# Optimization experiments

Hardware: AMD Instinct MI355X
Metric: run time of the kernel (lower is better)

Reference implementation:

```python
import jax, jax.numpy as jnp
import numpy as np
from jax import lax

EOS_ID = 2
START_ID = 1
NEG = -1e9
BEAM = 4
OUT_LEN = 48


def _lstm_gates(z):
    i, f, g, o = jnp.split(z, 4, axis=-1)
    return jax.nn.sigmoid(i), jax.nn.sigmoid(f), jnp.tanh(g), jax.nn.sigmoid(o)


def setup_inputs() -> dict:
    V, E, H, A = 32000, 512, 512, 512
    B, S_IN = 32, 128
    key = jax.random.key(0)
    ks = jax.random.split(key, 16)
    sd = 0.05
    n = lambda k, shp: jax.random.normal(k, shp, dtype=jnp.float32) * sd
    return {
        "encoder_inputs": jax.random.randint(ks[0], (B, S_IN), 0, V, dtype=jnp.int32),
        "decoder_inputs": jax.random.randint(ks[1], (B, OUT_LEN), 0, V, dtype=jnp.int32),
        "enc_emb": n(ks[2], (V, E)),
        "dec_emb": n(ks[3], (V, E)),
        "W_enc": n(ks[4], (E, 4 * H)),
        "U_enc": n(ks[5], (H, 4 * H)),
        "b_enc": jnp.zeros((4 * H,), jnp.float32),
        "W_dec": n(ks[6], (E + A, 4 * H)),
        "U_dec": n(ks[7], (H, 4 * H)),
        "b_dec": jnp.zeros((4 * H,), jnp.float32),
        "W_mem": n(ks[8], (H, A)),      # LuongAttention memory layer (no bias)
        "W_attn": n(ks[9], (2 * H, A)), # AttentionWrapper attention layer (no bias)
        "W_out": n(ks[10], (A, V)),
        "b_out": jnp.zeros((V,), jnp.float32),
    }


def reference(encoder_inputs, decoder_inputs, enc_emb, dec_emb, W_enc, U_enc, b_enc,
              W_dec, U_dec, b_dec, W_mem, W_attn, W_out, b_out):
    B = encoder_inputs.shape[0]
    H = U_enc.shape[0]
    A = W_mem.shape[1]
    V = W_out.shape[1]

    # ---- encoder LSTM (Keras gate order i,f,g,o) ----
    x = enc_emb[encoder_inputs]  # [B,S,E]
    def enc_step(carry, xt):
        h, c = carry
        i, f, g, o = _lstm_gates(xt @ W_enc + h @ U_enc + b_enc)
        c = f * c + i * g
        h = o * jnp.tanh(c)
        return (h, c), h
    h0 = jnp.zeros((B, H), x.dtype)
    (hN, cN), enc_out = lax.scan(enc_step, (h0, h0), x.transpose(1, 0, 2))
    enc_out = enc_out.transpose(1, 0, 2)       # [B,S,H] = attention values
    keys_mem = enc_out @ W_mem                 # [B,S,A] = attention keys

    # ---- beam search init (tile encoder final state over beams) ----
    h = jnp.broadcast_to(hN[:, None], (B, BEAM, H))
    c = jnp.broadcast_to(cN[:, None], (B, BEAM, H))
    attn = jnp.zeros((B, BEAM, A), x.dtype)
    cum = jnp.full((B, BEAM), NEG, x.dtype).at[:, 0].set(0.0)
    finished = jnp.zeros((B, BEAM), bool)
    tok = jnp.full((B, BEAM), START_ID, jnp.int32)
    eos_lp = jnp.full((V,), NEG, x.dtype).at[EOS_ID].set(0.0)

    def dec_step(carry, _):
        h, c, attn, cum, finished, tok = carry
        xe = dec_emb[tok]                                     # [B,K,E]
        inp = jnp.concatenate([xe, attn], axis=-1)            # cell_input_fn: concat(input, attention)
        i, f, g, o = _lstm_gates(inp @ W_dec + h @ U_dec + b_dec)
        c_new = f * c + i * g
        cell_out = o * jnp.tanh(c_new)                        # [B,K,H]
        scores = jnp.einsum('bkh,bsh->bks', cell_out, keys_mem)  # Luong dot score
        align = jax.nn.softmax(scores, axis=-1)
        ctx = jnp.einsum('bks,bsh->bkh', align, enc_out)
        attn_new = jnp.concatenate([cell_out, ctx], axis=-1) @ W_attn  # attention layer
        logits = attn_new @ W_out + b_out                     # [B,K,V]
        lp = jax.nn.log_softmax(logits, axis=-1)
        lp = jnp.where(finished[..., None], eos_lp, lp)       # finished beams repeat EOS
        total = cum[..., None] + lp
        vals, idx = lax.top_k(total.reshape(B, -1), BEAM)     # over K*V candidates
        parent = idx // V
        new_tok = (idx % V).astype(jnp.int32)
        g3 = lambda t: jnp.take_along_axis(t, parent[..., None], axis=1)
        h2 = g3(cell_out)
        c2 = g3(c_new)
        attn2 = g3(attn_new)
        fin = jnp.take_along_axis(finished, parent, axis=1) | (new_tok == EOS_ID)
        return (h2, c2, attn2, vals, fin, new_tok), (parent, new_tok)

    _, (parents, toks) = lax.scan(dec_step, (h, c, attn, cum, finished, tok), None, length=OUT_LEN)

    # ---- gather_tree: backtrack beam ancestry ----
    def back(ptr, pt):
        p, t = pt
        sel = jnp.take_along_axis(t, ptr, axis=1)
        return jnp.take_along_axis(p, ptr, axis=1), sel
    ptr0 = jnp.broadcast_to(jnp.arange(BEAM, dtype=jnp.int32)[None], (B, BEAM))
    _, pred = lax.scan(back, ptr0, (parents, toks), reverse=True)
    return pred.transpose(1, 0, 2)  # predicted_ids [B, T, beam]
```

## Files before the change

### kernel.cpp

```cpp
#include <hip/hip_runtime.h>
#include <math.h>

#define EOS_ID 2
#define START_ID 1
#define NEGV (-1e9f)

__device__ __forceinline__ float sigmoidf_(float x) { return 1.f / (1.f + expf(-x)); }

__device__ __forceinline__ void merge4_(float lv[4], int lc[4],
                                        const float rv[4], const int rc[4]) {
    float ov[4]; int oc[4];
    int ai = 0, bi = 0;
    #pragma unroll
    for (int o = 0; o < 4; o++) {
        const float avv = (ai == 0) ? lv[0] : (ai == 1) ? lv[1] : (ai == 2) ? lv[2] : lv[3];
        const int   acc = (ai == 0) ? lc[0] : (ai == 1) ? lc[1] : (ai == 2) ? lc[2] : lc[3];
        const float bvv = (bi == 0) ? rv[0] : (bi == 1) ? rv[1] : (bi == 2) ? rv[2] : rv[3];
        const int   bcc = (bi == 0) ? rc[0] : (bi == 1) ? rc[1] : (bi == 2) ? rc[2] : rc[3];
        const bool ta = (avv > bvv) || (avv == bvv && acc < bcc);
        ov[o] = ta ? avv : bvv;
        oc[o] = ta ? acc : bcc;
        if (ta) ai++; else bi++;
    }
    #pragma unroll
    for (int o = 0; o < 4; o++) { lv[o] = ov[o]; lc[o] = oc[o]; }
}

__device__ __forceinline__ void lse_combine_(float& m, float& s, float m2, float s2) {
    const float M = fmaxf(m, m2);
    s = s * expf(m - M) + s2 * expf(m2 - M);
    m = M;
}

template<int BM, int BN, int BK, int AMODE, int TRANS>
__global__ void __launch_bounds__(256) gemm_k(
    const float* __restrict__ A, const float* __restrict__ B,
    const float* __restrict__ bias, float* __restrict__ C,
    int M, int N, int K, const int* __restrict__ tokp)
{
    static_assert(BN == 64, "");
    constexpr int TM = BM / 16, TN = BN / 16;
    __shared__ __align__(16) float As[BK][BM];
    __shared__ __align__(16) float Bs[BK][BN];
    const int tid = threadIdx.x;
    const int n0 = blockIdx.x * BN, m0 = blockIdx.y * BM;
    const int tx = tid & 15, ty = tid >> 4;
    (void)M;

    float acc[TM][TN];
    #pragma unroll
    for (int i = 0; i < TM; i++)
        #pragma unroll
        for (int j = 0; j < TN; j++) acc[i][j] = 0.f;

    constexpr int A4 = BM * BK / 4;
    const bool aP = (A4 >= 256) || (tid < A4);
    const int am = tid / (BK / 4), ak4 = tid % (BK / 4);
    const int bk = tid >> 4, bn4 = tid & 15;

    const float* aRow = nullptr;
    if (aP) {
        if (AMODE == 0) {
            aRow = A + (size_t)(m0 + am) * K;
        } else {
            const int r = m0 + am;
            const int s = r >> 5, bidx = r & 31;
            aRow = A + (size_t)tokp[bidx * 128 + s] * 512;
        }
    }

    float4 aPF{}, bPF;
    if (aP) aPF = *reinterpret_cast<const float4*>(aRow + ak4 * 4);
    bPF = *reinterpret_cast<const float4*>(B + (size_t)bk * N + n0 + bn4 * 4);

    for (int k0 = 0; k0 < K; k0 += BK) {
        if (aP) {
            As[ak4 * 4 + 0][am] = aPF.x;
            As[ak4 * 4 + 1][am] = aPF.y;
            As[ak4 * 4 + 2][am] = aPF.z;
            As[ak4 * 4 + 3][am] = aPF.w;
        }
        *reinterpret_cast<float4*>(&Bs[bk][bn4 * 4]) = bPF;
        __syncthreads();
        const int kn = k0 + BK;
        if (kn < K) {
            if (aP) aPF = *reinterpret_cast<const float4*>(aRow + kn + ak4 * 4);
            bPF = *reinterpret_cast<const float4*>(B + (size_t)(kn + bk) * N + n0 + bn4 * 4);
        }
        #pragma unroll
        for (int kk = 0; kk < BK; kk++) {
            float af[TM], bf[TN];
            if constexpr (TM == 4) {
                const float4 t4 = *reinterpret_cast<const float4*>(&As[kk][ty * TM]);
                af[0] = t4.x; af[1] = t4.y; af[2] = t4.z; af[3] = t4.w;
            } else if constexpr (TM == 2) {
                const float2 t2 = *reinterpret_cast<const float2*>(&As[kk][ty * TM]);
                af[0] = t2.x; af[1] = t2.y;
            } else {
                af[0] = As[kk][ty];
            }
            const float4 b4 = *reinterpret_cast<const float4*>(&Bs[kk][tx * TN]);
            bf[0] = b4.x; bf[1] = b4.y; bf[2] = b4.z; bf[3] = b4.w;
            #pragma unroll
            for (int i = 0; i < TM; i++)
                #pragma unroll
                for (int j = 0; j < TN; j++) acc[i][j] += af[i] * bf[j];
        }
        __syncthreads();
    }

    if constexpr (TRANS) {
        #pragma unroll
        for (int i = 0; i < TM; i++) {
            const int r = m0 + ty * TM + i;
            const int b = r >> 7, s = r & 127;
            #pragma unroll
            for (int j = 0; j < TN; j++)
                C[((size_t)b * 512 + (n0 + tx * TN + j)) * 128 + s] = acc[i][j];
        }
    } else {
        float bv[TN];
        #pragma unroll
        for (int j = 0; j < TN; j++) bv[j] = bias ? bias[n0 + tx * TN + j] : 0.f;
        #pragma unroll
        for (int i = 0; i < TM; i++) {
            float4 o;
            o.x = acc[i][0] + bv[0]; o.y = acc[i][1] + bv[1];
            o.z = acc[i][2] + bv[2]; o.w = acc[i][3] + bv[3];
            *reinterpret_cast<float4*>(C + (size_t)(m0 + ty * TM + i) * N + n0 + tx * TN) = o;
        }
    }
}

__global__ void __launch_bounds__(256) pack_dec_k(
    const float* __restrict__ W_dec, const float* __restrict__ U_dec,
    const float* __restrict__ b_dec, float* __restrict__ Bp, float* __restrict__ bp,
    float* __restrict__ enc_c, float* __restrict__ hzero)
{
    const int idx = blockIdx.x * 256 + threadIdx.x;
    if (idx < 1536 * 2048) {
        const int k = idx >> 11, cp = idx & 2047;
        const int j = cp >> 2, g = cp & 3;
        const int sc = g * 512 + j;
        Bp[idx] = (k < 1024) ? W_dec[(size_t)k * 2048 + sc]
                             : U_dec[(size_t)(k - 1024) * 2048 + sc];
        if (idx < 2048) bp[idx] = b_dec[sc];
    }
    if (idx < 32 * 512) enc_c[idx] = 0.f;
    if (idx < 512) hzero[idx] = 0.f;
}

__global__ void __launch_bounds__(256) enc_step_k(
    const float* __restrict__ Xz_t, const float* __restrict__ hprev, long hstride,
    const float* __restrict__ U, float* __restrict__ c, float* __restrict__ hout)
{
    __shared__ __align__(16) float hs[512][2];
    __shared__ __align__(16) float zp[8][2][128];
    __shared__ float zfin[2][32][4];
    const int tid = threadIdx.x;
    const int jt = blockIdx.x;
    const int b0 = blockIdx.y * 2;

    {
        const int bb = tid >> 7, k4 = tid & 127;
        const float4 hv = *reinterpret_cast<const float4*>(
            hprev + (size_t)(b0 + bb) * hstride + k4 * 4);
        hs[k4 * 4 + 0][bb] = hv.x; hs[k4 * 4 + 1][bb] = hv.y;
        hs[k4 * 4 + 2][bb] = hv.z; hs[k4 * 4 + 3][bb] = hv.w;
    }
    __syncthreads();

    {
        const int kp = tid >> 5, cq = tid & 31;
        const int g = cq >> 3, j4 = (cq & 7) * 4;
        const int col = g * 512 + jt * 32 + j4;
        const int kbase = kp * 64;
        float4 A0 = {0.f, 0.f, 0.f, 0.f}, A1 = {0.f, 0.f, 0.f, 0.f};
        #pragma unroll 8
        for (int k = 0; k < 64; k++) {
            const float4 u4 = *reinterpret_cast<const float4*>(
                U + (size_t)(kbase + k) * 2048 + col);
            const float2 h2 = *reinterpret_cast<const float2*>(&hs[kbase + k][0]);
            A0.x += h2.x * u4.x; A0.y += h2.x * u4.y;
            A0.z += h2.x * u4.z; A0.w += h2.x * u4.w;
            A1.x += h2.y * u4.x; A1.y += h2.y * u4.y;
            A1.z += h2.y * u4.z; A1.w += h2.y * u4.w;
        }
        *reinterpret_cast<float4*>(&zp[kp][0][g * 32 + j4]) = A0;
        *reinterpret_cast<float4*>(&zp[kp][1][g * 32 + j4]) = A1;
    }
    __syncthreads();

    {
        const int bb = tid >> 7, rem = tid & 127;
        const int jj = rem >> 2, gg = rem & 3;
        float s = 0.f;
        #pragma unroll
        for (int p = 0; p < 8; p++) s += zp[p][bb][gg * 32 + jj];
        s += Xz_t[(size_t)(b0 + bb) * 2048 + gg * 512 + jt * 32 + jj];
        zfin[bb][jj][gg] = s;
    }
    __syncthreads();

    if (tid < 64) {
        const int bb = tid >> 5, jj = tid & 31;
        const int b = b0 + bb;
        const float iv = sigmoidf_(zfin[bb][jj][0]);
        const float fv = sigmoidf_(zfin[bb][jj][1]);
        const float gv = tanhf(zfin[bb][jj][2]);
        const float ov = sigmoidf_(zfin[bb][jj][3]);
        const int jglob = jt * 32 + jj;
        const size_t ci = (size_t)b * 512 + jglob;
        const float cv = fv * c[ci] + iv * gv;
        c[ci] = cv;
        hout[(size_t)b * 128 * 512 + jglob] = ov * tanhf(cv);
    }
}

__global__ void __launch_bounds__(256) init_dec_k(
    const float* __restrict__ enc_out, const float* __restrict__ enc_c,
    float* __restrict__ h_buf, float* __restrict__ c_buf, float* __restrict__ attn_buf,
    float* __restrict__ cum, int* __restrict__ fin, int* __restrict__ tok)
{
    const int idx = blockIdx.x * 256 + threadIdx.x;
    const int r = idx >> 9, jcol = idx & 511;
    const int b = r >> 2, kbeam = r & 3;
    h_buf[idx] = enc_out[((size_t)b * 128 + 127) * 512 + jcol];
    c_buf[idx] = enc_c[(size_t)b * 512 + jcol];
    attn_buf[idx] = 0.f;
    if (jcol == 0) {
        cum[r] = (kbeam == 0) ? 0.f : NEGV;
        fin[r] = 0;
        tok[r] = START_ID;
    }
}

__global__ void __launch_bounds__(256) zgemm_gates_k(
    const float* __restrict__ dec_emb, const float* __restrict__ Bp,
    const float* __restrict__ bp, const int* __restrict__ tok,
    const float* __restrict__ attn_buf, const float* __restrict__ h_buf,
    const float* __restrict__ c_buf, float* __restrict__ c_new,
    float* __restrict__ Acat)
{
    constexpr int BK = 16;
    __shared__ __align__(16) float As[BK][16];
    __shared__ __align__(16) float Bs[BK][64];
    const int tid = threadIdx.x;
    const int n0 = blockIdx.x * 64, m0 = blockIdx.y * 16;
    const int tx = tid & 15, ty = tid >> 4;

    float acc[4] = {0.f, 0.f, 0.f, 0.f};

    const bool aP = tid < 64;
    const int am = tid >> 2, ak4 = tid & 3;
    const int r = m0 + am;
    const int bk = tid >> 4, bn4 = tid & 15;
    const float* embRow = aP ? (dec_emb + (size_t)tok[r] * 512) : nullptr;

    auto loadA = [&](int k0) -> float4 {
        const int kg = k0 + ak4 * 4;
        if (kg < 512)
            return *reinterpret_cast<const float4*>(embRow + kg);
        if (kg < 1024)
            return *reinterpret_cast<const float4*>(attn_buf + (size_t)r * 512 + (kg - 512));
        return *reinterpret_cast<const float4*>(h_buf + (size_t)r * 512 + (kg - 1024));
    };

    float4 aPF{}, bPF;
    if (aP) aPF = loadA(0);
    bPF = *reinterpret_cast<const float4*>(Bp + (size_t)bk * 2048 + n0 + bn4 * 4);

    for (int k0 = 0; k0 < 1536; k0 += BK) {
        if (aP) {
            As[ak4 * 4 + 0][am] = aPF.x;
            As[ak4 * 4 + 1][am] = aPF.y;
            As[ak4 * 4 + 2][am] = aPF.z;
            As[ak4 * 4 + 3][am] = aPF.w;
        }
        *reinterpret_cast<float4*>(&Bs[bk][bn4 * 4]) = bPF;
        __syncthreads();
        const int kn = k0 + BK;
        if (kn < 1536) {
            if (aP) aPF = loadA(kn);
            bPF = *reinterpret_cast<const float4*>(Bp + (size_t)(kn + bk) * 2048 + n0 + bn4 * 4);
        }
        #pragma unroll
        for (int kk = 0; kk < BK; kk++) {
            const float a = As[kk][ty];
            const float4 b4 = *reinterpret_cast<const float4*>(&Bs[kk][tx * 4]);
            acc[0] += a * b4.x; acc[1] += a * b4.y;
            acc[2] += a * b4.z; acc[3] += a * b4.w;
        }
        __syncthreads();
    }

    const int rr = m0 + ty;
    const int j = (n0 >> 2) + tx;
    const float iv = sigmoidf_(acc[0] + bp[n0 + tx * 4 + 0]);
    const float fv = sigmoidf_(acc[1] + bp[n0 + tx * 4 + 1]);
    const float gv = tanhf   (acc[2] + bp[n0 + tx * 4 + 2]);
    const float ov = sigmoidf_(acc[3] + bp[n0 + tx * 4 + 3]);
    const float cv = fv * c_buf[(size_t)rr * 512 + j] + iv * gv;
    c_new[(size_t)rr * 512 + j] = cv;
    Acat[(size_t)rr * 1024 + j] = ov * tanhf(cv);
}

__global__ void __launch_bounds__(256) attention_k(
    const float* __restrict__ Acat, const float* __restrict__ keysT,
    const float* __restrict__ enc_out, float* __restrict__ AcatW)
{
    __shared__ __align__(16) float q[512];
    __shared__ float scp[2][128];
    __shared__ float sc[128];
    __shared__ float red[128];
    const int r = blockIdx.x;
    const int b = r >> 2;
    const int tid = threadIdx.x;

    if (tid < 128)
        reinterpret_cast<float4*>(q)[tid] =
            reinterpret_cast<const float4*>(Acat + (size_t)r * 1024)[tid];
    __syncthreads();

    {
        const int half = tid >> 7, s = tid & 127;
        const float* kp = keysT + ((size_t)b * 512 + half * 256) * 128 + s;
        float acc = 0.f;
        #pragma unroll 8
        for (int kk = 0; kk < 256; kk++) acc += q[half * 256 + kk] * kp[(size_t)kk * 128];
        scp[half][s] = acc;
    }
    __syncthreads();
    if (tid < 128) sc[tid] = scp[0][tid] + scp[1][tid];
    __syncthreads();
    if (tid < 64) red[tid] = fmaxf(sc[tid], sc[tid + 64]);
    __syncthreads();
    for (int st = 32; st >= 1; st >>= 1) {
        if (tid < st) red[tid] = fmaxf(red[tid], red[tid + st]);
        __syncthreads();
    }
    const float m = red[0];
    __syncthreads();
    if (tid < 128) sc[tid] = expf(sc[tid] - m);
    __syncthreads();
    if (tid < 64) red[tid] = sc[tid] + sc[tid + 64];
    __syncthreads();
    for (int st = 32; st >= 1; st >>= 1) {
        if (tid < st) red[tid] += red[tid + st];
        __syncthreads();
    }
    const float S = red[0];
    __syncthreads();
    if (tid < 128) sc[tid] = sc[tid] / S;
    __syncthreads();

    float a0 = 0.f, a1 = 0.f;
    for (int s = 0; s < 128; s++) {
        const float w = sc[s];
        const float* vr = enc_out + ((size_t)b * 128 + s) * 512;
        a0 += w * vr[tid];
        a1 += w * vr[tid + 256];
    }
    AcatW[(size_t)r * 1024 + 512 + tid] = a0;
    AcatW[(size_t)r * 1024 + 512 + tid + 256] = a1;
}

__global__ void __launch_bounds__(256) logits_top_k(
    const float* __restrict__ A, const float* __restrict__ B,
    const float* __restrict__ bias, float* __restrict__ pmax,
    float* __restrict__ psum, float* __restrict__ pval, int* __restrict__ pcol)
{
    constexpr int BK = 16;
    __shared__ __align__(16) float As[BK][128];
    __shared__ __align__(16) float Bs[BK][64];
    const int tid = threadIdx.x;
    const int n0 = blockIdx.x * 64;
    const int t = blockIdx.x;
    const int tx = tid & 15, ty = tid >> 4;

    float acc[8][4];
    #pragma unroll
    for (int i = 0; i < 8; i++)
        #pragma unroll
        for (int j = 0; j < 4; j++) acc[i][j] = 0.f;

    const int amA = tid >> 2, ak4 = tid & 3;
    const int bkB = tid >> 4, bn4 = tid & 15;

    float4 aPF0 = *reinterpret_cast<const float4*>(A + (size_t)amA * 512 + ak4 * 4);
    float4 aPF1 = *reinterpret_cast<const float4*>(A + (size_t)(64 + amA) * 512 + ak4 * 4);
    float4 bPF  = *reinterpret_cast<const float4*>(B + (size_t)bkB * 32000 + n0 + bn4 * 4);

    for (int k0 = 0; k0 < 512; k0 += BK) {
        As[ak4 * 4 + 0][amA] = aPF0.x;
        As[ak4 * 4 + 1][amA] = aPF0.y;
        As[ak4 * 4 + 2][amA] = aPF0.z;
        As[ak4 * 4 + 3][amA] = aPF0.w;
        As[ak4 * 4 + 0][64 + amA] = aPF1.x;
        As[ak4 * 4 + 1][64 + amA] = aPF1.y;
        As[ak4 * 4 + 2][64 + amA] = aPF1.z;
        As[ak4 * 4 + 3][64 + amA] = aPF1.w;
        *reinterpret_cast<float4*>(&Bs[bkB][bn4 * 4]) = bPF;
        __syncthreads();
        const int kn = k0 + BK;
        if (kn < 512) {
            aPF0 = *reinterpret_cast<const float4*>(A + (size_t)amA * 512 + kn + ak4 * 4);
            aPF1 = *reinterpret_cast<const float4*>(A + (size_t)(64 + amA) * 512 + kn + ak4 * 4);
            bPF  = *reinterpret_cast<const float4*>(B + (size_t)(kn + bkB) * 32000 + n0 + bn4 * 4);
        }
        #pragma unroll
        for (int kk = 0; kk < BK; kk++) {
            float af[8];
            const float4 t0 = *reinterpret_cast<const float4*>(&As[kk][ty * 8]);
            const float4 t1 = *reinterpret_cast<const float4*>(&As[kk][ty * 8 + 4]);
            af[0] = t0.x; af[1] = t0.y; af[2] = t0.z; af[3] = t0.w;
            af[4] = t1.x; af[5] = t1.y; af[6] = t1.z; af[7] = t1.w;
            const float4 b4 = *reinterpret_cast<const float4*>(&Bs[kk][tx * 4]);
            #pragma unroll
            for (int i = 0; i < 8; i++) {
                acc[i][0] += af[i] * b4.x; acc[i][1] += af[i] * b4.y;
                acc[i][2] += af[i] * b4.z; acc[i][3] += af[i] * b4.w;
            }
        }
        __syncthreads();
    }

    float bv[4];
    #pragma unroll
    for (int j = 0; j < 4; j++) bv[j] = bias[n0 + tx * 4 + j];

    #pragma unroll
    for (int i = 0; i < 8; i++) {
        const int r = ty * 8 + i;
        float lv[4]; int lc[4];
        #pragma unroll
        for (int j = 0; j < 4; j++) { lv[j] = acc[i][j] + bv[j]; lc[j] = n0 + tx * 4 + j; }
        float rm = fmaxf(fmaxf(lv[0], lv[1]), fmaxf(lv[2], lv[3]));
        #pragma unroll
        for (int d = 1; d <= 8; d <<= 1) rm = fmaxf(rm, __shfl_xor(rm, d));
        float s4 = expf(lv[0] - rm) + expf(lv[1] - rm) + expf(lv[2] - rm) + expf(lv[3] - rm);
        #pragma unroll
        for (int d = 1; d <= 8; d <<= 1) s4 += __shfl_xor(s4, d);
        #pragma unroll
        for (int p = 0; p < 3; p++)
            #pragma unroll
            for (int q = 0; q < 3 - p; q++)
                if (lv[q + 1] > lv[q]) {
                    const float tv = lv[q]; lv[q] = lv[q + 1]; lv[q + 1] = tv;
                    const int tc = lc[q]; lc[q] = lc[q + 1]; lc[q + 1] = tc;
                }
        #pragma unroll
        for (int d = 1; d <= 8; d <<= 1) {
            float rv[4]; int rc[4];
            #pragma unroll
            for (int j = 0; j < 4; j++) {
                rv[j] = __shfl_xor(lv[j], d);
                rc[j] = __shfl_xor(lc[j], d);
            }
            merge4_(lv, lc, rv, rc);
        }
        if (tx == 0) {
            pmax[r * 512 + t] = rm;
            psum[r * 512 + t] = s4;
            #pragma unroll
            for (int j = 0; j < 4; j++) {
                pval[(r * 4 + j) * 512 + t] = lv[j];
                pcol[(r * 4 + j) * 512 + t] = lc[j];
            }
        }
    }
}

__global__ void __launch_bounds__(1024) merge_update_k(
    const float* __restrict__ pmax, const float* __restrict__ psum,
    const float* __restrict__ pval, const int* __restrict__ pcol,
    float* __restrict__ cum, int* __restrict__ fin, int* __restrict__ tok,
    const float* __restrict__ Acat, const float* __restrict__ c_new,
    const float* __restrict__ attn_new,
    float* __restrict__ h_buf, float* __restrict__ c_buf, float* __restrict__ attn_buf,
    int* __restrict__ parents_t, int* __restrict__ toks_t)
{
    const int b = blockIdx.x;
    const int tid = threadIdx.x;
    const int rloc = tid >> 8, lt = tid & 255;
    const int r = b * 4 + rloc;

    __shared__ float sm[4][256], ss[4][256];
    __shared__ float sv[4][256][4];
    __shared__ int   sc4[4][256][4];
    __shared__ float rowlse[4], rowv[4][4];
    __shared__ int   rowc[4][4];
    __shared__ float oldcum[4];
    __shared__ int   oldfin[4], par[4];

    if (tid < 4) {
        oldcum[tid] = cum[b * 4 + tid];
        oldfin[tid] = fin[b * 4 + tid];
    }

    float m = -INFINITY, s = 0.f;
    float lv[4] = {-INFINITY, -INFINITY, -INFINITY, -INFINITY};
    int lc[4] = {0x7FFFFFFF, 0x7FFFFFFF, 0x7FFFFFFF, 0x7FFFFFFF};
    for (int t = lt; t < 500; t += 256) {
        lse_combine_(m, s, pmax[r * 512 + t], psum[r * 512 + t]);
        float rv[4]; int rc[4];
        #pragma unroll
        for (int j = 0; j < 4; j++) {
            rv[j] = pval[(r * 4 + j) * 512 + t];
            rc[j] = pcol[(r * 4 + j) * 512 + t];
        }
        merge4_(lv, lc, rv, rc);
    }
    sm[rloc][lt] = m; ss[rloc][lt] = s;
    #pragma unroll
    for (int j = 0; j < 4; j++) { sv[rloc][lt][j] = lv[j]; sc4[rloc][lt][j] = lc[j]; }
    __syncthreads();

    for (int st = 128; st >= 1; st >>= 1) {
        if (lt < st) {
            float m2 = sm[rloc][lt + st], s2 = ss[rloc][lt + st];
            lse_combine_(m, s, m2, s2);
            sm[rloc][lt] = m; ss[rloc][lt] = s;
            float rv[4]; int rc[4];
            #pragma unroll
            for (int j = 0; j < 4; j++) {
                rv[j] = sv[rloc][lt + st][j];
                rc[j] = sc4[rloc][lt + st][j];
            }
            merge4_(lv, lc, rv, rc);
            #pragma unroll
            for (int j = 0; j < 4; j++) { sv[rloc][lt][j] = lv[j]; sc4[rloc][lt][j] = lc[j]; }
        }
        __syncthreads();
    }
    if (lt == 0) {
        rowlse[rloc] = m + logf(s);
        #pragma unroll
        for (int j = 0; j < 4; j++) { rowv[rloc][j] = lv[j]; rowc[rloc][j] = lc[j]; }
    }
    __syncthreads();

    if (tid == 0) {
        float cv[16]; int ci[16];
        const int fillv[3] = {0, 1, 3};
        for (int k = 0; k < 4; k++) {
            if (oldfin[k]) {
                cv[k * 4 + 0] = oldcum[k];
                ci[k * 4 + 0] = k * 32000 + EOS_ID;
                for (int j = 1; j < 4; j++) {
                    cv[k * 4 + j] = oldcum[k] + NEGV;
                    ci[k * 4 + j] = k * 32000 + fillv[j - 1];
                }
            } else {
                const float lse = rowlse[k];
                for (int j = 0; j < 4; j++) {
                    cv[k * 4 + j] = oldcum[k] + (rowv[k][j] - lse);
                    ci[k * 4 + j] = k * 32000 + rowc[k][j];
                }
            }
        }
        for (int rr = 0; rr < 4; rr++) {
            float bvv = -INFINITY; int bix = 0x7FFFFFFF, bp_ = -1;
            for (int q = 0; q < 16; q++) {
                if (cv[q] > bvv || (cv[q] == bvv && ci[q] < bix)) {
                    bvv = cv[q]; bix = ci[q]; bp_ = q;
                }
            }
            cv[bp_] = -INFINITY; ci[bp_] = 0x7FFFFFFF;
            const int k = bix / 32000, v = bix - k * 32000;
            par[rr] = k;
            parents_t[b * 4 + rr] = k;
            toks_t[b * 4 + rr] = v;
            cum[b * 4 + rr] = bvv;
            tok[b * 4 + rr] = v;
            fin[b * 4 + rr] = (oldfin[k] || v == EOS_ID) ? 1 : 0;
        }
    }
    __syncthreads();

    for (int idx = tid; idx < 4 * 512; idx += 1024) {
        const int j = idx >> 9, col = idx & 511;
        const int sr = b * 4 + par[j], dr = b * 4 + j;
        h_buf[(size_t)dr * 512 + col] = Acat[(size_t)sr * 1024 + col];
        c_buf[(size_t)dr * 512 + col] = c_new[(size_t)sr * 512 + col];
        attn_buf[(size_t)dr * 512 + col] = attn_new[(size_t)sr * 512 + col];
    }
}

__global__ void __launch_bounds__(128) backtrack_k(
    const int* __restrict__ parents, const int* __restrict__ toks,
    int* __restrict__ out)
{
    const int tid = threadIdx.x;
    const int b = tid >> 2, kc = tid & 3;
    int ptr = kc;
    for (int t = 47; t >= 0; --t) {
        out[b * 192 + t * 4 + kc] = toks[t * 128 + b * 4 + ptr];
        ptr = parents[t * 128 + b * 4 + ptr];
    }
}

extern "C" void kernel_launch(void* const* d_in, const int* in_sizes, int n_in,
                              void* d_out, int out_size, void* d_ws, size_t ws_size,
                              hipStream_t stream)
{
    (void)in_sizes; (void)n_in; (void)out_size; (void)ws_size;
    const int* enc_in = (const int*)d_in[0];
    const float* enc_emb = (const float*)d_in[2];
    const float* dec_emb = (const float*)d_in[3];
    const float* W_enc = (const float*)d_in[4];
    const float* U_enc = (const float*)d_in[5];
    const float* b_enc = (const float*)d_in[6];
    const float* W_dec = (const float*)d_in[7];
    const float* U_dec = (const float*)d_in[8];
    const float* b_dec = (const float*)d_in[9];
    const float* W_mem = (const float*)d_in[10];
    const float* W_attn = (const float*)d_in[11];
    const float* W_out = (const float*)d_in[12];
    const float* b_out = (const float*)d_in[13];
    int* out = (int*)d_out;

    char* ws = (char*)d_ws;
    size_t off = 0;
    auto alloc = [&](size_t bytes) -> char* {
        char* p = ws + off;
        off = (off + bytes + 255) & ~(size_t)255;
        return p;
    };
    float* Xz       = (float*)alloc(128ull * 32 * 2048 * 4);
    float* enc_out  = (float*)alloc(32ull * 128 * 512 * 4);
    float* keysT    = (float*)alloc(32ull * 512 * 128 * 4);
    float* Bp       = (float*)alloc(1536ull * 2048 * 4);
    float* bp       = (float*)alloc(2048 * 4);
    float* enc_c    = (float*)alloc(32ull * 512 * 4);
    float* hzero    = (float*)alloc(512 * 4);
    float* h_buf    = (float*)alloc(128ull * 512 * 4);
    float* c_buf    = (float*)alloc(128ull * 512 * 4);
    float* attn_buf = (float*)alloc(128ull * 512 * 4);
    float* c_new    = (float*)alloc(128ull * 512 * 4);
    float* Acat     = (float*)alloc(128ull * 1024 * 4);
    float* attn_new = (float*)alloc(128ull * 512 * 4);
    float* pmax     = (float*)alloc(128ull * 512 * 4);
    float* psum     = (float*)alloc(128ull * 512 * 4);
    float* pval     = (float*)alloc(512ull * 512 * 4);
    int*   pcol     = (int*)alloc(512ull * 512 * 4);
    float* cum      = (float*)alloc(128 * 4);
    int* fin        = (int*)alloc(128 * 4);
    int* tok        = (int*)alloc(128 * 4);
    int* parents    = (int*)alloc(48 * 128 * 4);
    int* toks       = (int*)alloc(48 * 128 * 4);

    pack_dec_k<<<(1536 * 2048) / 256, 256, 0, stream>>>(W_dec, U_dec, b_dec, Bp, bp,
                                                        enc_c, hzero);

    gemm_k<64, 64, 16, 2, 0><<<dim3(32, 64), 256, 0, stream>>>(
        enc_emb, W_enc, b_enc, Xz, 4096, 2048, 512, enc_in);

    for (int t = 0; t < 128; t++) {
        const float* hprev = t ? (enc_out + (size_t)(t - 1) * 512) : hzero;
        const long hstride = t ? (long)(128 * 512) : 0;
        enc_step_k<<<dim3(16, 16), 256, 0, stream>>>(
            Xz + (size_t)t * 32 * 2048, hprev, hstride, U_enc, enc_c,
            enc_out + (size_t)t * 512);
    }

    gemm_k<64, 64, 16, 0, 1><<<dim3(8, 64), 256, 0, stream>>>(
        enc_out, W_mem, nullptr, keysT, 4096, 512, 512, nullptr);

    init_dec_k<<<256, 256, 0, stream>>>(enc_out, enc_c, h_buf, c_buf, attn_buf,
                                        cum, fin, tok);

    for (int t = 0; t < 48; t++) {
        zgemm_gates_k<<<dim3(32, 8), 256, 0, stream>>>(
            dec_emb, Bp, bp, tok, attn_buf, h_buf, c_buf, c_new, Acat);
        attention_k<<<128, 256, 0, stream>>>(Acat, keysT, enc_out, Acat);
        gemm_k<16, 64, 16, 0, 0><<<dim3(8, 8), 256, 0, stream>>>(
            Acat, W_attn, nullptr, attn_new, 128, 512, 1024, nullptr);
        logits_top_k<<<500, 256, 0, stream>>>(
            attn_new, W_out, b_out, pmax, psum, pval, pcol);
        merge_update_k<<<32, 1024, 0, stream>>>(
            pmax, psum, pval, pcol, cum, fin, tok, Acat, c_new, attn_new,
            h_buf, c_buf, attn_buf, parents + t * 128, toks + t * 128);
    }

    backtrack_k<<<1, 128, 0, stream>>>(parents, toks, out);
}
```

Before: 10.87 ms.

## Replace per-step kernel launches with persistent kernels using grid barriers

The 128 encoder step launches become one persistent kernel of 128 blocks, each handling 4 batch rows, with a software grid barrier between timesteps. The 240 per-step decoder launches become one persistent kernel of 512 blocks that runs gates, attention, projection, logits/top-k and the beam merge as phases separated by grid barriers. This removes launch overhead and inter-kernel gaps on a latency-bound recurrent workload. It relies on all blocks being co-resident, and the spin barrier has a timeout that can silently break ordering. It also adds defensive clamps on token and parent indices.

```diff
diff --git a/kernel.cpp b/kernel.cpp
--- a/kernel.cpp
+++ b/kernel.cpp
@@ -32,6 +32,25 @@
     m = M;
 }
 
+__device__ __forceinline__ void gsync_(int* bar, int nb, int& g, bool& dead) {
+    __syncthreads();
+    if (threadIdx.x == 0 && !dead) {
+        __threadfence();
+        if (atomicAdd(&bar[0], 1) == nb - 1) {
+            atomicExch(&bar[0], 0);
+            __hip_atomic_store(&bar[1], g + 1, __ATOMIC_RELEASE, __HIP_MEMORY_SCOPE_AGENT);
+        } else {
+            int sp = 0;
+            while (__hip_atomic_load(&bar[1], __ATOMIC_RELAXED, __HIP_MEMORY_SCOPE_AGENT) - g <= 0) {
+                if (++sp > (1 << 22)) { dead = true; break; }
+            }
+            __threadfence();
+        }
+        g++;
+    }
+    __syncthreads();
+}
+
 template<int BM, int BN, int BK, int AMODE, int TRANS>
 __global__ void __launch_bounds__(256) gemm_k(
     const float* __restrict__ A, const float* __restrict__ B,
@@ -135,7 +154,8 @@
 __global__ void __launch_bounds__(256) pack_dec_k(
     const float* __restrict__ W_dec, const float* __restrict__ U_dec,
     const float* __restrict__ b_dec, float* __restrict__ Bp, float* __restrict__ bp,
-    float* __restrict__ enc_c, float* __restrict__ hzero)
+    float* __restrict__ enc_c, float* __restrict__ hzero,
+    int* __restrict__ barA, int* __restrict__ barB)
 {
     const int idx = blockIdx.x * 256 + threadIdx.x;
     if (idx < 1536 * 2048) {
@@ -148,72 +168,88 @@
     }
     if (idx < 32 * 512) enc_c[idx] = 0.f;
     if (idx < 512) hzero[idx] = 0.f;
-}
-
-__global__ void __launch_bounds__(256) enc_step_k(
-    const float* __restrict__ Xz_t, const float* __restrict__ hprev, long hstride,
-    const float* __restrict__ U, float* __restrict__ c, float* __restrict__ hout)
+    if (idx == 0) { barA[0] = 0; barA[1] = 0; barB[0] = 0; barB[1] = 0; }
+}
+
+__global__ void __launch_bounds__(256, 1) enc_persist_k(
+    const float* __restrict__ Xz, const float* __restrict__ hzero,
+    const float* __restrict__ U, float* __restrict__ c,
+    float* __restrict__ enc_out, int* __restrict__ bar)
 {
-    __shared__ __align__(16) float hs[512][2];
-    __shared__ __align__(16) float zp[8][2][128];
-    __shared__ float zfin[2][32][4];
+    __shared__ __align__(16) float hs[512][4];
+    __shared__ __align__(16) float zp[8][4][128];
+    __shared__ float zfin[4][32][4];
     const int tid = threadIdx.x;
-    const int jt = blockIdx.x;
-    const int b0 = blockIdx.y * 2;
-
-    {
-        const int bb = tid >> 7, k4 = tid & 127;
-        const float4 hv = *reinterpret_cast<const float4*>(
-            hprev + (size_t)(b0 + bb) * hstride + k4 * 4);
-        hs[k4 * 4 + 0][bb] = hv.x; hs[k4 * 4 + 1][bb] = hv.y;
-        hs[k4 * 4 + 2][bb] = hv.z; hs[k4 * 4 + 3][bb] = hv.w;
-    }
-    __syncthreads();
-
-    {
-        const int kp = tid >> 5, cq = tid & 31;
-        const int g = cq >> 3, j4 = (cq & 7) * 4;
-        const int col = g * 512 + jt * 32 + j4;
-        const int kbase = kp * 64;
-        float4 A0 = {0.f, 0.f, 0.f, 0.f}, A1 = {0.f, 0.f, 0.f, 0.f};
-        #pragma unroll 8
-        for (int k = 0; k < 64; k++) {
-            const float4 u4 = *reinterpret_cast<const float4*>(
-                U + (size_t)(kbase + k) * 2048 + col);
-            const float2 h2 = *reinterpret_cast<const float2*>(&hs[kbase + k][0]);
-            A0.x += h2.x * u4.x; A0.y += h2.x * u4.y;
-            A0.z += h2.x * u4.z; A0.w += h2.x * u4.w;
-            A1.x += h2.y * u4.x; A1.y += h2.y * u4.y;
-            A1.z += h2.y * u4.z; A1.w += h2.y * u4.w;
-        }
-        *reinterpret_cast<float4*>(&zp[kp][0][g * 32 + j4]) = A0;
-        *reinterpret_cast<float4*>(&zp[kp][1][g * 32 + j4]) = A1;
-    }
-    __syncthreads();
-
-    {
-        const int bb = tid >> 7, rem = tid & 127;
-        const int jj = rem >> 2, gg = rem & 3;
-        float s = 0.f;
+    const int jt = blockIdx.x & 15;
+    const int b0 = (blockIdx.x >> 4) * 4;
+    int gen = 0; bool dead = false;
+
+    for (int t = 0; t < 128; t++) {
+        const float* hprev = t ? (enc_out + (size_t)(t - 1) * 512) : hzero;
+        const long hstride = t ? (long)(128 * 512) : 0;
+
         #pragma unroll
-        for (int p = 0; p < 8; p++) s += zp[p][bb][gg * 32 + jj];
-        s += Xz_t[(size_t)(b0 + bb) * 2048 + gg * 512 + jt * 32 + jj];
-        zfin[bb][jj][gg] = s;
-    }
-    __syncthreads();
-
-    if (tid < 64) {
-        const int bb = tid >> 5, jj = tid & 31;
-        const int b = b0 + bb;
-        const float iv = sigmoidf_(zfin[bb][jj][0]);
-        const float fv = sigmoidf_(zfin[bb][jj][1]);
-        const float gv = tanhf(zfin[bb][jj][2]);
-        const float ov = sigmoidf_(zfin[bb][jj][3]);
-        const int jglob = jt * 32 + jj;
-        const size_t ci = (size_t)b * 512 + jglob;
-        const float cv = fv * c[ci] + iv * gv;
-        c[ci] = cv;
-        hout[(size_t)b * 128 * 512 + jglob] = ov * tanhf(cv);
+        for (int i2 = 0; i2 < 2; i2++) {
+            const int idx = tid + i2 * 256;
+            const int bb = idx >> 7, k4 = idx & 127;
+            const float4 hv = *reinterpret_cast<const float4*>(
+                hprev + (size_t)(b0 + bb) * hstride + k4 * 4);
+            hs[k4 * 4 + 0][bb] = hv.x; hs[k4 * 4 + 1][bb] = hv.y;
+            hs[k4 * 4 + 2][bb] = hv.z; hs[k4 * 4 + 3][bb] = hv.w;
+        }
+        __syncthreads();
+
+        {
+            const int kp = tid >> 5, cq = tid & 31;
+            const int g = cq >> 3, j4 = (cq & 7) * 4;
+            const int col = g * 512 + jt * 32 + j4;
+            const int kbase = kp * 64;
+            float4 A0 = {0.f,0.f,0.f,0.f}, A1 = {0.f,0.f,0.f,0.f};
+            float4 A2 = {0.f,0.f,0.f,0.f}, A3 = {0.f,0.f,0.f,0.f};
+            #pragma unroll 8
+            for (int k = 0; k < 64; k++) {
+                const float4 u4 = *reinterpret_cast<const float4*>(
+                    U + (size_t)(kbase + k) * 2048 + col);
+                const float4 h4 = *reinterpret_cast<const float4*>(&hs[kbase + k][0]);
+                A0.x += h4.x * u4.x; A0.y += h4.x * u4.y; A0.z += h4.x * u4.z; A0.w += h4.x * u4.w;
+                A1.x += h4.y * u4.x; A1.y += h4.y * u4.y; A1.z += h4.y * u4.z; A1.w += h4.y * u4.w;
+                A2.x += h4.z * u4.x; A2.y += h4.z * u4.y; A2.z += h4.z * u4.z; A2.w += h4.z * u4.w;
+                A3.x += h4.w * u4.x; A3.y += h4.w * u4.y; A3.z += h4.w * u4.z; A3.w += h4.w * u4.w;
+            }
+            *reinterpret_cast<float4*>(&zp[kp][0][g * 32 + j4]) = A0;
+            *reinterpret_cast<float4*>(&zp[kp][1][g * 32 + j4]) = A1;
+            *reinterpret_cast<float4*>(&zp[kp][2][g * 32 + j4]) = A2;
+            *reinterpret_cast<float4*>(&zp[kp][3][g * 32 + j4]) = A3;
+        }
+        __syncthreads();
+
+        #pragma unroll
+        for (int i2 = 0; i2 < 2; i2++) {
+            const int idx = tid + i2 * 256;
+            const int bb = idx >> 7, rem = idx & 127;
+            const int jj = rem >> 2, gg2 = rem & 3;
+            float s = 0.f;
+            #pragma unroll
+            for (int p = 0; p < 8; p++) s += zp[p][bb][gg2 * 32 + jj];
+            s += Xz[(size_t)t * 32 * 2048 + (size_t)(b0 + bb) * 2048 + gg2 * 512 + jt * 32 + jj];
+            zfin[bb][jj][gg2] = s;
+        }
+        __syncthreads();
+
+        if (tid < 128) {
+            const int bb = tid >> 5, jj = tid & 31;
+            const int b = b0 + bb;
+            const float iv = sigmoidf_(zfin[bb][jj][0]);
+            const float fv = sigmoidf_(zfin[bb][jj][1]);
+            const float gv = tanhf(zfin[bb][jj][2]);
+            const float ov = sigmoidf_(zfin[bb][jj][3]);
+            const int jglob = jt * 32 + jj;
+            const size_t ci = (size_t)b * 512 + jglob;
+            const float cv = fv * c[ci] + iv * gv;
+            c[ci] = cv;
+            enc_out[(size_t)b * 128 * 512 + (size_t)t * 512 + jglob] = ov * tanhf(cv);
+        }
+        gsync_(bar, 128, gen, dead);
     }
 }
 
@@ -235,355 +271,393 @@
     }
 }
 
-__global__ void __launch_bounds__(256) zgemm_gates_k(
+struct __align__(16) SDec {
+    union {
+        struct { float As[16][16];  float Bs[16][64]; } g;
+        struct { float q[512]; float scp[2][128]; float sc[128]; float red[128]; } a;
+        struct { float As[16][128]; float Bs[16][64]; } l;
+        struct { float sm[256]; float ss[256]; float sv[256][4]; int sci[256][4]; } m;
+    } u;
+    int par[4];
+};
+
+#define NB_DEC 512
+
+__global__ void __launch_bounds__(256, 2) dec_persist_k(
     const float* __restrict__ dec_emb, const float* __restrict__ Bp,
-    const float* __restrict__ bp, const int* __restrict__ tok,
-    const float* __restrict__ attn_buf, const float* __restrict__ h_buf,
-    const float* __restrict__ c_buf, float* __restrict__ c_new,
-    float* __restrict__ Acat)
+    const float* __restrict__ bp, int* __restrict__ tok,
+    float* __restrict__ attn_buf, float* __restrict__ h_buf,
+    float* __restrict__ c_buf, float* __restrict__ c_new,
+    float* __restrict__ Acat, const float* __restrict__ keysT,
+    const float* __restrict__ enc_out, const float* __restrict__ W_attn,
+    float* __restrict__ attn_new, const float* __restrict__ W_out,
+    const float* __restrict__ b_out, float* __restrict__ pmax,
+    float* __restrict__ psum, float* __restrict__ pval, int* __restrict__ pcol,
+    float* __restrict__ cum, int* __restrict__ fin,
+    int* __restrict__ parents, int* __restrict__ toks,
+    float* __restrict__ rowlse_g, float* __restrict__ rowv_g, int* __restrict__ rowc_g,
+    int* __restrict__ bar)
 {
-    constexpr int BK = 16;
-    __shared__ __align__(16) float As[BK][16];
-    __shared__ __align__(16) float Bs[BK][64];
+    __shared__ SDec S;
     const int tid = threadIdx.x;
-    const int n0 = blockIdx.x * 64, m0 = blockIdx.y * 16;
+    const int bid = blockIdx.x;
     const int tx = tid & 15, ty = tid >> 4;
-
-    float acc[4] = {0.f, 0.f, 0.f, 0.f};
-
-    const bool aP = tid < 64;
-    const int am = tid >> 2, ak4 = tid & 3;
-    const int r = m0 + am;
-    const int bk = tid >> 4, bn4 = tid & 15;
-    const float* embRow = aP ? (dec_emb + (size_t)tok[r] * 512) : nullptr;
-
-    auto loadA = [&](int k0) -> float4 {
-        const int kg = k0 + ak4 * 4;
-        if (kg < 512)
-            return *reinterpret_cast<const float4*>(embRow + kg);
-        if (kg < 1024)
-            return *reinterpret_cast<const float4*>(attn_buf + (size_t)r * 512 + (kg - 512));
-        return *reinterpret_cast<const float4*>(h_buf + (size_t)r * 512 + (kg - 1024));
-    };
-
-    float4 aPF{}, bPF;
-    if (aP) aPF = loadA(0);
-    bPF = *reinterpret_cast<const float4*>(Bp + (size_t)bk * 2048 + n0 + bn4 * 4);
-
-    for (int k0 = 0; k0 < 1536; k0 += BK) {
-        if (aP) {
-            As[ak4 * 4 + 0][am] = aPF.x;
-            As[ak4 * 4 + 1][am] = aPF.y;
-            As[ak4 * 4 + 2][am] = aPF.z;
-            As[ak4 * 4 + 3][am] = aPF.w;
-        }
-        *reinterpret_cast<float4*>(&Bs[bk][bn4 * 4]) = bPF;
-        __syncthreads();
-        const int kn = k0 + BK;
-        if (kn < 1536) {
-            if (aP) aPF = loadA(kn);
-            bPF = *reinterpret_cast<const float4*>(Bp + (size_t)(kn + bk) * 2048 + n0 + bn4 * 4);
-        }
-        #pragma unroll
-        for (int kk = 0; kk < BK; kk++) {
-            const float a = As[kk][ty];
-            const float4 b4 = *reinterpret_cast<const float4*>(&Bs[kk][tx * 4]);
-            acc[0] += a * b4.x; acc[1] += a * b4.y;
-            acc[2] += a * b4.z; acc[3] += a * b4.w;
-        }
-        __syncthreads();
-    }
-
-    const int rr = m0 + ty;
-    const int j = (n0 >> 2) + tx;
-    const float iv = sigmoidf_(acc[0] + bp[n0 + tx * 4 + 0]);
-    const float fv = sigmoidf_(acc[1] + bp[n0 + tx * 4 + 1]);
-    const float gv = tanhf   (acc[2] + bp[n0 + tx * 4 + 2]);
-    const float ov = sigmoidf_(acc[3] + bp[n0 + tx * 4 + 3]);
-    const float cv = fv * c_buf[(size_t)rr * 512 + j] + iv * gv;
-    c_new[(size_t)rr * 512 + j] = cv;
-    Acat[(size_t)rr * 1024 + j] = ov * tanhf(cv);
-}
-
-__global__ void __launch_bounds__(256) attention_k(
-    const float* __restrict__ Acat, const float* __restrict__ keysT,
-    const float* __restrict__ enc_out, float* __restrict__ AcatW)
-{
-    __shared__ __align__(16) float q[512];
-    __shared__ float scp[2][128];
-    __shared__ float sc[128];
-    __shared__ float red[128];
-    const int r = blockIdx.x;
-    const int b = r >> 2;
-    const int tid = threadIdx.x;
-
-    if (tid < 128)
-        reinterpret_cast<float4*>(q)[tid] =
-            reinterpret_cast<const float4*>(Acat + (size_t)r * 1024)[tid];
-    __syncthreads();
-
-    {
-        const int half = tid >> 7, s = tid & 127;
-        const float* kp = keysT + ((size_t)b * 512 + half * 256) * 128 + s;
-        float acc = 0.f;
-        #pragma unroll 8
-        for (int kk = 0; kk < 256; kk++) acc += q[half * 256 + kk] * kp[(size_t)kk * 128];
-        scp[half][s] = acc;
-    }
-    __syncthreads();
-    if (tid < 128) sc[tid] = scp[0][tid] + scp[1][tid];
-    __syncthreads();
-    if (tid < 64) red[tid] = fmaxf(sc[tid], sc[tid + 64]);
-    __syncthreads();
-    for (int st = 32; st >= 1; st >>= 1) {
-        if (tid < st) red[tid] = fmaxf(red[tid], red[tid + st]);
-        __syncthreads();
-    }
-    const float m = red[0];
-    __syncthreads();
-    if (tid < 128) sc[tid] = expf(sc[tid] - m);
-    __syncthreads();
-    if (tid < 64) red[tid] = sc[tid] + sc[tid + 64];
-    __syncthreads();
-    for (int st = 32; st >= 1; st >>= 1) {
-        if (tid < st) red[tid] += red[tid + st];
-        __syncthreads();
-    }
-    const float S = red[0];
-    __syncthreads();
-    if (tid < 128) sc[tid] = sc[tid] / S;
-    __syncthreads();
-
-    float a0 = 0.f, a1 = 0.f;
-    for (int s = 0; s < 128; s++) {
-        const float w = sc[s];
-        const float* vr = enc_out + ((size_t)b * 128 + s) * 512;
-        a0 += w * vr[tid];
-        a1 += w * vr[tid + 256];
-    }
-    AcatW[(size_t)r * 1024 + 512 + tid] = a0;
-    AcatW[(size_t)r * 1024 + 512 + tid + 256] = a1;
-}
-
-__global__ void __launch_bounds__(256) logits_top_k(
-    const float* __restrict__ A, const float* __restrict__ B,
-    const float* __restrict__ bias, float* __restrict__ pmax,
-    float* __restrict__ psum, float* __restrict__ pval, int* __restrict__ pcol)
-{
-    constexpr int BK = 16;
-    __shared__ __align__(16) float As[BK][128];
-    __shared__ __align__(16) float Bs[BK][64];
-    const int tid = threadIdx.x;
-    const int n0 = blockIdx.x * 64;
-    const int t = blockIdx.x;
-    const int tx = tid & 15, ty = tid >> 4;
-
-    float acc[8][4];
-    #pragma unroll
-    for (int i = 0; i < 8; i++)
-        #pragma unroll
-        for (int j = 0; j < 4; j++) acc[i][j] = 0.f;
-
-    const int amA = tid >> 2, ak4 = tid & 3;
-    const int bkB = tid >> 4, bn4 = tid & 15;
-
-    float4 aPF0 = *reinterpret_cast<const float4*>(A + (size_t)amA * 512 + ak4 * 4);
-    float4 aPF1 = *reinterpret_cast<const float4*>(A + (size_t)(64 + amA) * 512 + ak4 * 4);
-    float4 bPF  = *reinterpret_cast<const float4*>(B + (size_t)bkB * 32000 + n0 + bn4 * 4);
-
-    for (int k0 = 0; k0 < 512; k0 += BK) {
-        As[ak4 * 4 + 0][amA] = aPF0.x;
-        As[ak4 * 4 + 1][amA] = aPF0.y;
-        As[ak4 * 4 + 2][amA] = aPF0.z;
-        As[ak4 * 4 + 3][amA] = aPF0.w;
-        As[ak4 * 4 + 0][64 + amA] = aPF1.x;
-        As[ak4 * 4 + 1][64 + amA] = aPF1.y;
-        As[ak4 * 4 + 2][64 + amA] = aPF1.z;
-        As[ak4 * 4 + 3][64 + amA] = aPF1.w;
-        *reinterpret_cast<float4*>(&Bs[bkB][bn4 * 4]) = bPF;
-        __syncthreads();
-        const int kn = k0 + BK;
-        if (kn < 512) {
-            aPF0 = *reinterpret_cast<const float4*>(A + (size_t)amA * 512 + kn + ak4 * 4);
-            aPF1 = *reinterpret_cast<const float4*>(A + (size_t)(64 + amA) * 512 + kn + ak4 * 4);
-            bPF  = *reinterpret_cast<const float4*>(B + (size_t)(kn + bkB) * 32000 + n0 + bn4 * 4);
-        }
-        #pragma unroll
-        for (int kk = 0; kk < BK; kk++) {
-            float af[8];
-            const float4 t0 = *reinterpret_cast<const float4*>(&As[kk][ty * 8]);
-            const float4 t1 = *reinterpret_cast<const float4*>(&As[kk][ty * 8 + 4]);
-            af[0] = t0.x; af[1] = t0.y; af[2] = t0.z; af[3] = t0.w;
-            af[4] = t1.x; af[5] = t1.y; af[6] = t1.z; af[7] = t1.w;
-            const float4 b4 = *reinterpret_cast<const float4*>(&Bs[kk][tx * 4]);
+    int gen = 0; bool dead = false;
+
+    for (int step = 0; step < 48; step++) {
+        if (bid < 256) {
+            const int n0 = (bid & 31) * 64, m0 = (bid >> 5) * 16;
+            float acc[4] = {0.f, 0.f, 0.f, 0.f};
+            const bool aP = tid < 64;
+            const int am = tid >> 2, ak4 = tid & 3;
+            const int r = m0 + am;
+            const int bk = tid >> 4, bn4 = tid & 15;
+            const float* embRow = nullptr;
+            if (aP) {
+                int tk = tok[r];
+                tk = (tk < 0) ? 0 : ((tk > 31999) ? 31999 : tk);
+                embRow = dec_emb + (size_t)tk * 512;
+            }
+
+            auto loadA = [&](int k0) -> float4 {
+                const int kg = k0 + ak4 * 4;
+                if (kg < 512)
+                    return *reinterpret_cast<const float4*>(embRow + kg);
+                if (kg < 1024)
+                    return *reinterpret_cast<const float4*>(attn_buf + (size_t)r * 512 + (kg - 512));
+                return *reinterpret_cast<const float4*>(h_buf + (size_t)r * 512 + (kg - 1024));
+            };
+
+            float4 aPF{}, bPF;
+            if (aP) aPF = loadA(0);
+            bPF = *reinterpret_cast<const float4*>(Bp + (size_t)bk * 2048 + n0 + bn4 * 4);
+
+            for (int k0 = 0; k0 < 1536; k0 += 16) {
+                if (aP) {
+                    S.u.g.As[ak4 * 4 + 0][am] = aPF.x;
+                    S.u.g.As[ak4 * 4 + 1][am] = aPF.y;
+                    S.u.g.As[ak4 * 4 + 2][am] = aPF.z;
+                    S.u.g.As[ak4 * 4 + 3][am] = aPF.w;
+                }
+                *reinterpret_cast<float4*>(&S.u.g.Bs[bk][bn4 * 4]) = bPF;
+                __syncthreads();
+                const int kn = k0 + 16;
+                if (kn < 1536) {
+                    if (aP) aPF = loadA(kn);
+                    bPF = *reinterpret_cast<const float4*>(Bp + (size_t)(kn + bk) * 2048 + n0 + bn4 * 4);
+                }
+                #pragma unroll
+                for (int kk = 0; kk < 16; kk++) {
+                    const float a = S.u.g.As[kk][ty];
+                    const float4 b4 = *reinterpret_cast<const float4*>(&S.u.g.Bs[kk][tx * 4]);
+                    acc[0] += a * b4.x; acc[1] += a * b4.y;
+                    acc[2] += a * b4.z; acc[3] += a * b4.w;
+                }
+                __syncthreads();
+            }
+
+            const int rr = m0 + ty;
+            const int j = (n0 >> 2) + tx;
+            const float iv = sigmoidf_(acc[0] + bp[n0 + tx * 4 + 0]);
+            const float fv = sigmoidf_(acc[1] + bp[n0 + tx * 4 + 1]);
+            const float gv = tanhf   (acc[2] + bp[n0 + tx * 4 + 2]);
+            const float ov = sigmoidf_(acc[3] + bp[n0 + tx * 4 + 3]);
+            const float cv = fv * c_buf[(size_t)rr * 512 + j] + iv * gv;
+            c_new[(size_t)rr * 512 + j] = cv;
+            Acat[(size_t)rr * 1024 + j] = ov * tanhf(cv);
+        }
+        gsync_(bar, NB_DEC, gen, dead);
+
+        if (bid < 128) {
+            const int r = bid;
+            const int b = r >> 2;
+
+            if (tid < 128)
+                reinterpret_cast<float4*>(S.u.a.q)[tid] =
+                    reinterpret_cast<const float4*>(Acat + (size_t)r * 1024)[tid];
+            __syncthreads();
+
+            {
+                const int half = tid >> 7, s = tid & 127;
+                const float* kp = keysT + ((size_t)b * 512 + half * 256) * 128 + s;
+                float acc = 0.f;
+                #pragma unroll 8
+                for (int kk = 0; kk < 256; kk++)
+                    acc += S.u.a.q[half * 256 + kk] * kp[(size_t)kk * 128];
+                S.u.a.scp[half][s] = acc;
+            }
+            __syncthreads();
+            if (tid < 128) S.u.a.sc[tid] = S.u.a.scp[0][tid] + S.u.a.scp[1][tid];
+            __syncthreads();
+            if (tid < 64) S.u.a.red[tid] = fmaxf(S.u.a.sc[tid], S.u.a.sc[tid + 64]);
+            __syncthreads();
+            for (int st = 32; st >= 1; st >>= 1) {
+                if (tid < st) S.u.a.red[tid] = fmaxf(S.u.a.red[tid], S.u.a.red[tid + st]);
+                __syncthreads();
+            }
+            const float m = S.u.a.red[0];
+            __syncthreads();
+            if (tid < 128) S.u.a.sc[tid] = expf(S.u.a.sc[tid] - m);
+            __syncthreads();
+            if (tid < 64) S.u.a.red[tid] = S.u.a.sc[tid] + S.u.a.sc[tid + 64];
+            __syncthreads();
+            for (int st = 32; st >= 1; st >>= 1) {
+                if (tid < st) S.u.a.red[tid] += S.u.a.red[tid + st];
+                __syncthreads();
+            }
+            const float Ssum = S.u.a.red[0];
+            __syncthreads();
+            if (tid < 128) S.u.a.sc[tid] = S.u.a.sc[tid] / Ssum;
+            __syncthreads();
+
+            float a0 = 0.f, a1 = 0.f;
+            for (int s = 0; s < 128; s++) {
+                const float w = S.u.a.sc[s];
+                const float* vr = enc_out + ((size_t)b * 128 + s) * 512;
+                a0 += w * vr[tid];
+                a1 += w * vr[tid + 256];
+            }
+            Acat[(size_t)r * 1024 + 512 + tid] = a0;
+            Acat[(size_t)r * 1024 + 512 + tid + 256] = a1;
+        }
+        gsync_(bar, NB_DEC, gen, dead);
+
+        if (bid < 64) {
+            const int n0 = (bid & 7) * 64, m0 = (bid >> 3) * 16;
+            float acc[4] = {0.f, 0.f, 0.f, 0.f};
+            const bool aP = tid < 64;
+            const int am = tid >> 2, ak4 = tid & 3;
+            const int bk = tid >> 4, bn4 = tid & 15;
+            const float* aRow = Acat + (size_t)(m0 + am) * 1024;
+
+            float4 aPF{}, bPF;
+            if (aP) aPF = *reinterpret_cast<const float4*>(aRow + ak4 * 4);
+            bPF = *reinterpret_cast<const float4*>(W_attn + (size_t)bk * 512 + n0 + bn4 * 4);
+
+            for (int k0 = 0; k0 < 1024; k0 += 16) {
+                if (aP) {
+                    S.u.g.As[ak4 * 4 + 0][am] = aPF.x;
+                    S.u.g.As[ak4 * 4 + 1][am] = aPF.y;
+                    S.u.g.As[ak4 * 4 + 2][am] = aPF.z;
+                    S.u.g.As[ak4 * 4 + 3][am] = aPF.w;
+                }
+                *reinterpret_cast<float4*>(&S.u.g.Bs[bk][bn4 * 4]) = bPF;
+                __syncthreads();
+                const int kn = k0 + 16;
+                if (kn < 1024) {
+                    if (aP) aPF = *reinterpret_cast<const float4*>(aRow + kn + ak4 * 4);
+                    bPF = *reinterpret_cast<const float4*>(W_attn + (size_t)(kn + bk) * 512 + n0 + bn4 * 4);
+                }
+                #pragma unroll
+                for (int kk = 0; kk < 16; kk++) {
+                    const float a = S.u.g.As[kk][ty];
+                    const float4 b4 = *reinterpret_cast<const float4*>(&S.u.g.Bs[kk][tx * 4]);
+                    acc[0] += a * b4.x; acc[1] += a * b4.y;
+                    acc[2] += a * b4.z; acc[3] += a * b4.w;
+                }
+                __syncthreads();
+            }
+            float4 o;
+            o.x = acc[0]; o.y = acc[1]; o.z = acc[2]; o.w = acc[3];
+            *reinterpret_cast<float4*>(attn_new + (size_t)(m0 + ty) * 512 + n0 + tx * 4) = o;
+        }
+        gsync_(bar, NB_DEC, gen, dead);
+
+        if (bid < 500) {
+            const int tile = bid;
+            const int n0 = tile * 64;
+            float acc[8][4];
+            #pragma unroll
+            for (int i = 0; i < 8; i++)
+                #pragma unroll
+                for (int j = 0; j < 4; j++) acc[i][j] = 0.f;
+
+            const int amA = tid >> 2, ak4 = tid & 3;
+            const int bkB = tid >> 4, bn4 = tid & 15;
+
+            float4 aPF0 = *reinterpret_cast<const float4*>(attn_new + (size_t)amA * 512 + ak4 * 4);
+            float4 aPF1 = *reinterpret_cast<const float4*>(attn_new + (size_t)(64 + amA) * 512 + ak4 * 4);
+            float4 bPF  = *reinterpret_cast<const float4*>(W_out + (size_t)bkB * 32000 + n0 + bn4 * 4);
+
+            for (int k0 = 0; k0 < 512; k0 += 16) {
+                S.u.l.As[ak4 * 4 + 0][amA] = aPF0.x;
+                S.u.l.As[ak4 * 4 + 1][amA] = aPF0.y;
+                S.u.l.As[ak4 * 4 + 2][amA] = aPF0.z;
+                S.u.l.As[ak4 * 4 + 3][amA] = aPF0.w;
+                S.u.l.As[ak4 * 4 + 0][64 + amA] = aPF1.x;
+                S.u.l.As[ak4 * 4 + 1][64 + amA] = aPF1.y;
+                S.u.l.As[ak4 * 4 + 2][64 + amA] = aPF1.z;
+                S.u.l.As[ak4 * 4 + 3][64 + amA] = aPF1.w;
+                *reinterpret_cast<float4*>(&S.u.l.Bs[bkB][bn4 * 4]) = bPF;
+                __syncthreads();
+                const int kn = k0 + 16;
+                if (kn < 512) {
+                    aPF0 = *reinterpret_cast<const float4*>(attn_new + (size_t)amA * 512 + kn + ak4 * 4);
+                    aPF1 = *reinterpret_cast<const float4*>(attn_new + (size_t)(64 + amA) * 512 + kn + ak4 * 4);
+                    bPF  = *reinterpret_cast<const float4*>(W_out + (size_t)(kn + bkB) * 32000 + n0 + bn4 * 4);
+                }
+                #pragma unroll
+                for (int kk = 0; kk < 16; kk++) {
+                    float af[8];
+                    const float4 t0 = *reinterpret_cast<const float4*>(&S.u.l.As[kk][ty * 8]);
+                    const float4 t1 = *reinterpret_cast<const float4*>(&S.u.l.As[kk][ty * 8 + 4]);
+                    af[0] = t0.x; af[1] = t0.y; af[2] = t0.z; af[3] = t0.w;
+                    af[4] = t1.x; af[5] = t1.y; af[6] = t1.z; af[7] = t1.w;
+                    const float4 b4 = *reinterpret_cast<const float4*>(&S.u.l.Bs[kk][tx * 4]);
+                    #pragma unroll
+                    for (int i = 0; i < 8; i++) {
+                        acc[i][0] += af[i] * b4.x; acc[i][1] += af[i] * b4.y;
+                        acc[i][2] += af[i] * b4.z; acc[i][3] += af[i] * b4.w;
+                    }
+                }
+                __syncthreads();
+            }
+
+            float bv[4];
+            #pragma unroll
+            for (int j = 0; j < 4; j++) bv[j] = b_out[n0 + tx * 4 + j];
+
             #pragma unroll
             for (int i = 0; i < 8; i++) {
-                acc[i][0] += af[i] * b4.x; acc[i][1] += af[i] * b4.y;
-                acc[i][2] += af[i] * b4.z; acc[i][3] += af[i] * b4.w;
-            }
-        }
-        __syncthreads();
-    }
-
-    float bv[4];
-    #pragma unroll
-    for (int j = 0; j < 4; j++) bv[j] = bias[n0 + tx * 4 + j];
-
-    #pragma unroll
-    for (int i = 0; i < 8; i++) {
-        const int r = ty * 8 + i;
-        float lv[4]; int lc[4];
-        #pragma unroll
-        for (int j = 0; j < 4; j++) { lv[j] = acc[i][j] + bv[j]; lc[j] = n0 + tx * 4 + j; }
-        float rm = fmaxf(fmaxf(lv[0], lv[1]), fmaxf(lv[2], lv[3]));
-        #pragma unroll
-        for (int d = 1; d <= 8; d <<= 1) rm = fmaxf(rm, __shfl_xor(rm, d));
-        float s4 = expf(lv[0] - rm) + expf(lv[1] - rm) + expf(lv[2] - rm) + expf(lv[3] - rm);
-        #pragma unroll
-        for (int d = 1; d <= 8; d <<= 1) s4 += __shfl_xor(s4, d);
-        #pragma unroll
-        for (int p = 0; p < 3; p++)
+                const int r = ty * 8 + i;
+                float lv[4]; int lc[4];
+                #pragma unroll
+                for (int j = 0; j < 4; j++) { lv[j] = acc[i][j] + bv[j]; lc[j] = n0 + tx * 4 + j; }
+                float rm = fmaxf(fmaxf(lv[0], lv[1]), fmaxf(lv[2], lv[3]));
+                #pragma unroll
+                for (int d = 1; d <= 8; d <<= 1) rm = fmaxf(rm, __shfl_xor(rm, d));
+                float s4 = expf(lv[0] - rm) + expf(lv[1] - rm) + expf(lv[2] - rm) + expf(lv[3] - rm);
+                #pragma unroll
+                for (int d = 1; d <= 8; d <<= 1) s4 += __shfl_xor(s4, d);
+                #pragma unroll
+                for (int p = 0; p < 3; p++)
+                    #pragma unroll
+                    for (int q = 0; q < 3 - p; q++)
+                        if (lv[q + 1] > lv[q]) {
+                            const float tv = lv[q]; lv[q] = lv[q + 1]; lv[q + 1] = tv;
+                            const int tc = lc[q]; lc[q] = lc[q + 1]; lc[q + 1] = tc;
+                        }
+                #pragma unroll
+                for (int d = 1; d <= 8; d <<= 1) {
+                    float rv[4]; int rc[4];
+                    #pragma unroll
+                    for (int j = 0; j < 4; j++) {
+                        rv[j] = __shfl_xor(lv[j], d);
+                        rc[j] = __shfl_xor(lc[j], d);
+                    }
+                    merge4_(lv, lc, rv, rc);
+                }
+                if (tx == 0) {
+                    pmax[r * 512 + tile] = rm;
+                    psum[r * 512 + tile] = s4;
+                    #pragma unroll
+                    for (int j = 0; j < 4; j++) {
+                        pval[(r * 4 + j) * 512 + tile] = lv[j];
+                        pcol[(r * 4 + j) * 512 + tile] = lc[j];
+                    }
+                }
+            }
+        }
+        gsync_(bar, NB_DEC, gen, dead);
+
+        if (bid < 128) {
+            const int r = bid;
+            float m = -INFINITY, s = 0.f;
+            float lv[4] = {-INFINITY, -INFINITY, -INFINITY, -INFINITY};
+            int lc[4] = {0x7FFFFFFF, 0x7FFFFFFF, 0x7FFFFFFF, 0x7FFFFFFF};
+            for (int tt = tid; tt < 500; tt += 256) {
+                lse_combine_(m, s, pmax[r * 512 + tt], psum[r * 512 + tt]);
+                float rv[4]; int rc[4];
+                #pragma unroll
+                for (int j = 0; j < 4; j++) {
+                    rv[j] = pval[(r * 4 + j) * 512 + tt];
+                    rc[j] = pcol[(r * 4 + j) * 512 + tt];
+                }
+                merge4_(lv, lc, rv, rc);
+            }
+            S.u.m.sm[tid] = m; S.u.m.ss[tid] = s;
             #pragma unroll
-            for (int q = 0; q < 3 - p; q++)
-                if (lv[q + 1] > lv[q]) {
-                    const float tv = lv[q]; lv[q] = lv[q + 1]; lv[q + 1] = tv;
-                    const int tc = lc[q]; lc[q] = lc[q + 1]; lc[q + 1] = tc;
-                }
-        #pragma unroll
-        for (int d = 1; d <= 8; d <<= 1) {
-            float rv[4]; int rc[4];
-            #pragma unroll
-            for (int j = 0; j < 4; j++) {
-                rv[j] = __shfl_xor(lv[j], d);
-                rc[j] = __shfl_xor(lc[j], d);
-            }
-            merge4_(lv, lc, rv, rc);
-        }
-        if (tx == 0) {
-            pmax[r * 512 + t] = rm;
-            psum[r * 512 + t] = s4;
-            #pragma unroll
-            for (int j = 0; j < 4; j++) {
-                pval[(r * 4 + j) * 512 + t] = lv[j];
-                pcol[(r * 4 + j) * 512 + t] = lc[j];
-            }
-        }
-    }
-}
-
-__global__ void __launch_bounds__(1024) merge_update_k(
-    const float* __restrict__ pmax, const float* __restrict__ psum,
-    const float* __restrict__ pval, const int* __restrict__ pcol,
-    float* __restrict__ cum, int* __restrict__ fin, int* __restrict__ tok,
-    const float* __restrict__ Acat, const float* __restrict__ c_new,
-    const float* __restrict__ attn_new,
-    float* __restrict__ h_buf, float* __restrict__ c_buf, float* __restrict__ attn_buf,
-    int* __restrict__ parents_t, int* __restrict__ toks_t)
-{
-    const int b = blockIdx.x;
-    const int tid = threadIdx.x;
-    const int rloc = tid >> 8, lt = tid & 255;
-    const int r = b * 4 + rloc;
-
-    __shared__ float sm[4][256], ss[4][256];
-    __shared__ float sv[4][256][4];
-    __shared__ int   sc4[4][256][4];
-    __shared__ float rowlse[4], rowv[4][4];
-    __shared__ int   rowc[4][4];
-    __shared__ float oldcum[4];
-    __shared__ int   oldfin[4], par[4];
-
-    if (tid < 4) {
-        oldcum[tid] = cum[b * 4 + tid];
-        oldfin[tid] = fin[b * 4 + tid];
-    }
-
-    float m = -INFINITY, s = 0.f;
-    float lv[4] = {-INFINITY, -INFINITY, -INFINITY, -INFINITY};
-    int lc[4] = {0x7FFFFFFF, 0x7FFFFFFF, 0x7FFFFFFF, 0x7FFFFFFF};
-    for (int t = lt; t < 500; t += 256) {
-        lse_combine_(m, s, pmax[r * 512 + t], psum[r * 512 + t]);
-        float rv[4]; int rc[4];
-        #pragma unroll
-        for (int j = 0; j < 4; j++) {
-            rv[j] = pval[(r * 4 + j) * 512 + t];
-            rc[j] = pcol[(r * 4 + j) * 512 + t];
-        }
-        merge4_(lv, lc, rv, rc);
-    }
-    sm[rloc][lt] = m; ss[rloc][lt] = s;
-    #pragma unroll
-    for (int j = 0; j < 4; j++) { sv[rloc][lt][j] = lv[j]; sc4[rloc][lt][j] = lc[j]; }
-    __syncthreads();
-
-    for (int st = 128; st >= 1; st >>= 1) {
-        if (lt < st) {
-            float m2 = sm[rloc][lt + st], s2 = ss[rloc][lt + st];
-            lse_combine_(m, s, m2, s2);
-            sm[rloc][lt] = m; ss[rloc][lt] = s;
-            float rv[4]; int rc[4];
-            #pragma unroll
-            for (int j = 0; j < 4; j++) {
-                rv[j] = sv[rloc][lt + st][j];
-                rc[j] = sc4[rloc][lt + st][j];
-            }
-            merge4_(lv, lc, rv, rc);
-            #pragma unroll
-            for (int j = 0; j < 4; j++) { sv[rloc][lt][j] = lv[j]; sc4[rloc][lt][j] = lc[j]; }
-        }
-        __syncthreads();
-    }
-    if (lt == 0) {
-        rowlse[rloc] = m + logf(s);
-        #pragma unroll
-        for (int j = 0; j < 4; j++) { rowv[rloc][j] = lv[j]; rowc[rloc][j] = lc[j]; }
-    }
-    __syncthreads();
-
-    if (tid == 0) {
-        float cv[16]; int ci[16];
-        const int fillv[3] = {0, 1, 3};
-        for (int k = 0; k < 4; k++) {
-            if (oldfin[k]) {
-                cv[k * 4 + 0] = oldcum[k];
-                ci[k * 4 + 0] = k * 32000 + EOS_ID;
-                for (int j = 1; j < 4; j++) {
-                    cv[k * 4 + j] = oldcum[k] + NEGV;
-                    ci[k * 4 + j] = k * 32000 + fillv[j - 1];
-                }
-            } else {
-                const float lse = rowlse[k];
-                for (int j = 0; j < 4; j++) {
-                    cv[k * 4 + j] = oldcum[k] + (rowv[k][j] - lse);
-                    ci[k * 4 + j] = k * 32000 + rowc[k][j];
-                }
-            }
-        }
-        for (int rr = 0; rr < 4; rr++) {
-            float bvv = -INFINITY; int bix = 0x7FFFFFFF, bp_ = -1;
-            for (int q = 0; q < 16; q++) {
-                if (cv[q] > bvv || (cv[q] == bvv && ci[q] < bix)) {
-                    bvv = cv[q]; bix = ci[q]; bp_ = q;
-                }
-            }
-            cv[bp_] = -INFINITY; ci[bp_] = 0x7FFFFFFF;
-            const int k = bix / 32000, v = bix - k * 32000;
-            par[rr] = k;
-            parents_t[b * 4 + rr] = k;
-            toks_t[b * 4 + rr] = v;
-            cum[b * 4 + rr] = bvv;
-            tok[b * 4 + rr] = v;
-            fin[b * 4 + rr] = (oldfin[k] || v == EOS_ID) ? 1 : 0;
-        }
-    }
-    __syncthreads();
-
-    for (int idx = tid; idx < 4 * 512; idx += 1024) {
-        const int j = idx >> 9, col = idx & 511;
-        const int sr = b * 4 + par[j], dr = b * 4 + j;
-        h_buf[(size_t)dr * 512 + col] = Acat[(size_t)sr * 1024 + col];
-        c_buf[(size_t)dr * 512 + col] = c_new[(size_t)sr * 512 + col];
-        attn_buf[(size_t)dr * 512 + col] = attn_new[(size_t)sr * 512 + col];
+            for (int j = 0; j < 4; j++) { S.u.m.sv[tid][j] = lv[j]; S.u.m.sci[tid][j] = lc[j]; }
+            __syncthreads();
+
+            for (int st = 128; st >= 1; st >>= 1) {
+                if (tid < st) {
+                    lse_combine_(m, s, S.u.m.sm[tid + st], S.u.m.ss[tid + st]);
+                    S.u.m.sm[tid] = m; S.u.m.ss[tid] = s;
+                    float rv[4]; int rc[4];
+                    #pragma unroll
+                    for (int j = 0; j < 4; j++) {
+                        rv[j] = S.u.m.sv[tid + st][j];
+                        rc[j] = S.u.m.sci[tid + st][j];
+                    }
+                    merge4_(lv, lc, rv, rc);
+                    #pragma unroll
+                    for (int j = 0; j < 4; j++) { S.u.m.sv[tid][j] = lv[j]; S.u.m.sci[tid][j] = lc[j]; }
+                }
+                __syncthreads();
+            }
+            if (tid == 0) {
+                rowlse_g[r] = m + logf(s);
+                #pragma unroll
+                for (int j = 0; j < 4; j++) { rowv_g[r * 4 + j] = lv[j]; rowc_g[r * 4 + j] = lc[j]; }
+            }
+        }
+        gsync_(bar, NB_DEC, gen, dead);
+
+        if (bid < 32) {
+            const int b = bid;
+            if (tid == 0) {
+                float oldcum[4]; int oldfin[4];
+                for (int k = 0; k < 4; k++) {
+                    oldcum[k] = cum[b * 4 + k];
+                    oldfin[k] = fin[b * 4 + k];
+                }
+                float cv[16]; int ci[16];
+                const int fillv[3] = {0, 1, 3};
+                for (int k = 0; k < 4; k++) {
+                    if (oldfin[k]) {
+                        cv[k * 4 + 0] = oldcum[k];
+                        ci[k * 4 + 0] = k * 32000 + EOS_ID;
+                        for (int j = 1; j < 4; j++) {
+                            cv[k * 4 + j] = oldcum[k] + NEGV;
+                            ci[k * 4 + j] = k * 32000 + fillv[j - 1];
+                        }
+                    } else {
+                        const float lse = rowlse_g[b * 4 + k];
+                        for (int j = 0; j < 4; j++) {
+                            cv[k * 4 + j] = oldcum[k] + (rowv_g[(b * 4 + k) * 4 + j] - lse);
+                            ci[k * 4 + j] = k * 32000 + rowc_g[(b * 4 + k) * 4 + j];
+                        }
+                    }
+                }
+                for (int rr = 0; rr < 4; rr++) {
+                    float bvv = -INFINITY; int bix = 0x7FFFFFFF, bp_ = -1;
+                    for (int q = 0; q < 16; q++) {
+                        if (cv[q] > bvv || (cv[q] == bvv && ci[q] < bix)) {
+                            bvv = cv[q]; bix = ci[q]; bp_ = q;
+                        }
+                    }
+                    cv[bp_] = -INFINITY; ci[bp_] = 0x7FFFFFFF;
+                    const int k = (bix / 32000) & 3;
+                    const int v = bix - (bix / 32000) * 32000;
+                    S.par[rr] = k;
+                    parents[step * 128 + b * 4 + rr] = k;
+                    toks[step * 128 + b * 4 + rr] = v;
+                    cum[b * 4 + rr] = bvv;
+                    tok[b * 4 + rr] = v;
+                    fin[b * 4 + rr] = (oldfin[k] || v == EOS_ID) ? 1 : 0;
+                }
+            }
+            __syncthreads();
+            for (int idx = tid; idx < 4 * 512; idx += 256) {
+                const int j = idx >> 9, col = idx & 511;
+                const int sr = b * 4 + S.par[j], dr = b * 4 + j;
+                h_buf[(size_t)dr * 512 + col] = Acat[(size_t)sr * 1024 + col];
+                c_buf[(size_t)dr * 512 + col] = c_new[(size_t)sr * 512 + col];
+                attn_buf[(size_t)dr * 512 + col] = attn_new[(size_t)sr * 512 + col];
+            }
+        }
+        gsync_(bar, NB_DEC, gen, dead);
     }
 }
 
@@ -596,7 +670,7 @@
     int ptr = kc;
     for (int t = 47; t >= 0; --t) {
         out[b * 192 + t * 4 + kc] = toks[t * 128 + b * 4 + ptr];
-        ptr = parents[t * 128 + b * 4 + ptr];
+        ptr = parents[t * 128 + b * 4 + ptr] & 3;
     }
 }
 
@@ -649,20 +723,19 @@
     int* tok        = (int*)alloc(128 * 4);
     int* parents    = (int*)alloc(48 * 128 * 4);
     int* toks       = (int*)alloc(48 * 128 * 4);
+    float* rowlse_g = (float*)alloc(128 * 4);
+    float* rowv_g   = (float*)alloc(512 * 4);
+    int*   rowc_g   = (int*)alloc(512 * 4);
+    int*   barA     = (int*)alloc(256);
+    int*   barB     = (int*)alloc(256);
 
     pack_dec_k<<<(1536 * 2048) / 256, 256, 0, stream>>>(W_dec, U_dec, b_dec, Bp, bp,
-                                                        enc_c, hzero);
+                                                        enc_c, hzero, barA, barB);
 
     gemm_k<64, 64, 16, 2, 0><<<dim3(32, 64), 256, 0, stream>>>(
         enc_emb, W_enc, b_enc, Xz, 4096, 2048, 512, enc_in);
 
-    for (int t = 0; t < 128; t++) {
-        const float* hprev = t ? (enc_out + (size_t)(t - 1) * 512) : hzero;
-        const long hstride = t ? (long)(128 * 512) : 0;
-        enc_step_k<<<dim3(16, 16), 256, 0, stream>>>(
-            Xz + (size_t)t * 32 * 2048, hprev, hstride, U_enc, enc_c,
-            enc_out + (size_t)t * 512);
-    }
+    enc_persist_k<<<128, 256, 0, stream>>>(Xz, hzero, U_enc, enc_c, enc_out, barA);
 
     gemm_k<64, 64, 16, 0, 1><<<dim3(8, 64), 256, 0, stream>>>(
         enc_out, W_mem, nullptr, keysT, 4096, 512, 512, nullptr);
@@ -670,18 +743,10 @@
     init_dec_k<<<256, 256, 0, stream>>>(enc_out, enc_c, h_buf, c_buf, attn_buf,
                                         cum, fin, tok);
 
-    for (int t = 0; t < 48; t++) {
-        zgemm_gates_k<<<dim3(32, 8), 256, 0, stream>>>(
-            dec_emb, Bp, bp, tok, attn_buf, h_buf, c_buf, c_new, Acat);
-        attention_k<<<128, 256, 0, stream>>>(Acat, keysT, enc_out, Acat);
-        gemm_k<16, 64, 16, 0, 0><<<dim3(8, 8), 256, 0, stream>>>(
-            Acat, W_attn, nullptr, attn_new, 128, 512, 1024, nullptr);
-        logits_top_k<<<500, 256, 0, stream>>>(
-            attn_new, W_out, b_out, pmax, psum, pval, pcol);
-        merge_update_k<<<32, 1024, 0, stream>>>(
-            pmax, psum, pval, pcol, cum, fin, tok, Acat, c_new, attn_new,
-            h_buf, c_buf, attn_buf, parents + t * 128, toks + t * 128);
-    }
+    dec_persist_k<<<NB_DEC, 256, 0, stream>>>(
+        dec_emb, Bp, bp, tok, attn_buf, h_buf, c_buf, c_new, Acat, keysT,
+        enc_out, W_attn, attn_new, W_out, b_out, pmax, psum, pval, pcol,
+        cum, fin, parents, toks, rowlse_g, rowv_g, rowc_g, barB);
 
     backtrack_k<<<1, 128, 0, stream>>>(parents, toks, out);
 }
```

Measured after the change: 26.46 ms. 2.43x slower.
